# Kernel optimization log

Hardware: AMD Instinct MI355X
Metric: run time of the kernel (lower is better)

The kernel has to match this reference:

```python
import jax, jax.numpy as jnp
import numpy as np

D_MODEL = 1024
FFN_H = 4096
N_EXPERTS = 8
TOP_K = 2
AUX_COEFF = 0.01


def setup_inputs() -> dict:
    key = jax.random.key(0)
    k_x, k_r, k_w1, k_w2 = jax.random.split(key, 4)
    x = jax.random.normal(k_x, (2, 2048, D_MODEL), dtype=jnp.float32)
    Wr = jax.random.normal(k_r, (N_EXPERTS, D_MODEL), dtype=jnp.float32) * (D_MODEL ** -0.5)
    W1 = jax.random.normal(k_w1, (N_EXPERTS, FFN_H, D_MODEL), dtype=jnp.float32) * (D_MODEL ** -0.5)
    W2 = jax.random.normal(k_w2, (N_EXPERTS, D_MODEL, FFN_H), dtype=jnp.float32) * (FFN_H ** -0.5)
    return {"x": x, "Wr": Wr, "W1": W1, "W2": W2}


def reference(x, Wr, W1, W2):
    B, T, D = x.shape
    E = Wr.shape[0]
    x_flat = x.reshape(-1, D)  # (N, D)
    # Router: softmax over experts, top-k, renormalize
    router_logits = x_flat @ Wr.T  # (N, E)
    router_probs = jax.nn.softmax(router_logits, axis=-1)
    top_k_probs, top_k_indices = jax.lax.top_k(router_probs, TOP_K)
    top_k_probs = top_k_probs / (top_k_probs.sum(-1, keepdims=True) + 1e-8)
    # Dense all-expert FFN (faithful to the vectorized dispatch)
    h = jnp.einsum('nd,ehd->neh', x_flat, W1)  # (N, E, H)
    h = jax.nn.gelu(h, approximate=False)      # torch F.gelu default = erf
    out_all = jnp.einsum('neh,edh->ned', h, W2)  # (N, E, D)
    topk_out = jnp.take_along_axis(out_all, top_k_indices[:, :, None], axis=1)  # (N, K, D)
    output = (topk_out * top_k_probs[:, :, None]).sum(1)  # (N, D)
    # Load-balance aux loss (MSE to uniform)
    tokens_per_expert = router_probs.mean(0)
    aux_loss = AUX_COEFF * jnp.mean((tokens_per_expert - 1.0 / E) ** 2)
    return output.reshape(B, T, D), aux_loss
```

## Files before the change

kernel.cpp:

```cpp
#include <hip/hip_runtime.h>
#include <cstdint>
#include <cstddef>

#define N_TOK 4096
#define DM 1024
#define FH 4096
#define NE 8
#define MT_PAD 72

typedef __attribute__((ext_vector_type(8))) short short8;
typedef __attribute__((ext_vector_type(4))) float f32x4;

#define WAITV0() asm volatile("s_waitcnt vmcnt(0)" ::: "memory")

__device__ __forceinline__ unsigned short f2bf(float f) {
  unsigned u = __float_as_uint(f);
  u += 0x7fffu + ((u >> 16) & 1u);
  return (unsigned short)(u >> 16);
}

__device__ __forceinline__ float gelu_fast(float v) {
  float e = __expf(1.5957692f * v * fmaf(0.044715f, v * v, 1.0f));
  return v - v * __builtin_amdgcn_rcpf(1.0f + e);
}

__global__ void cvt_kernel(const float* __restrict__ src, unsigned short* __restrict__ dst, int n4) {
  int stride = gridDim.x * blockDim.x;
  for (int i = blockIdx.x * blockDim.x + threadIdx.x; i < n4; i += stride) {
    float4 v = reinterpret_cast<const float4*>(src)[i];
    ushort4 o;
    o.x = f2bf(v.x); o.y = f2bf(v.y); o.z = f2bf(v.z); o.w = f2bf(v.w);
    reinterpret_cast<ushort4*>(dst)[i] = o;
  }
}

__global__ void router_kernel(const float* __restrict__ x, const float* __restrict__ Wr,
                              float* __restrict__ partials, unsigned char* __restrict__ topidx,
                              float* __restrict__ pslot, unsigned short* __restrict__ xb) {
  __shared__ float sp[NE];
  int lane = threadIdx.x & 63;
  int wv = threadIdx.x >> 6;
  int token = blockIdx.x * 4 + wv;
  if (threadIdx.x < NE) sp[threadIdx.x] = 0.f;
  __syncthreads();

  const float4* xr = (const float4*)(x + (size_t)token * DM);
  ushort4* xw = (ushort4*)(xb + (size_t)token * DM);
  float acc[NE];
#pragma unroll
  for (int e = 0; e < NE; e++) acc[e] = 0.f;
#pragma unroll
  for (int d = lane; d < DM / 4; d += 64) {
    float4 xv = xr[d];
    ushort4 o;
    o.x = f2bf(xv.x); o.y = f2bf(xv.y); o.z = f2bf(xv.z); o.w = f2bf(xv.w);
    xw[d] = o;
#pragma unroll
    for (int e = 0; e < NE; e++) {
      float4 wv4 = ((const float4*)(Wr + e * DM))[d];
      acc[e] += xv.x * wv4.x + xv.y * wv4.y + xv.z * wv4.z + xv.w * wv4.w;
    }
  }
#pragma unroll
  for (int e = 0; e < NE; e++) {
#pragma unroll
    for (int off = 32; off > 0; off >>= 1) acc[e] += __shfl_xor(acc[e], off);
  }
  if (lane == 0) {
    float m = acc[0];
#pragma unroll
    for (int e = 1; e < NE; e++) m = fmaxf(m, acc[e]);
    float p[NE];
    float s = 0.f;
#pragma unroll
    for (int e = 0; e < NE; e++) { p[e] = expf(acc[e] - m); s += p[e]; }
    float inv = 1.f / s;
#pragma unroll
    for (int e = 0; e < NE; e++) p[e] *= inv;
    int i1 = 0;
#pragma unroll
    for (int e = 1; e < NE; e++) if (p[e] > p[i1]) i1 = e;
    int i2 = (i1 == 0) ? 1 : 0;
#pragma unroll
    for (int e = 0; e < NE; e++) if (e != i1 && p[e] > p[i2]) i2 = e;
    float denom = p[i1] + p[i2] + 1e-8f;
    topidx[token] = (unsigned char)(i1 | (i2 << 4));
    pslot[2 * token]     = p[i1] / denom;
    pslot[2 * token + 1] = p[i2] / denom;
#pragma unroll
    for (int e = 0; e < NE; e++) atomicAdd(&sp[e], p[e]);
  }
  __syncthreads();
  if (threadIdx.x < NE) partials[blockIdx.x * NE + threadIdx.x] = sp[threadIdx.x];
}

__global__ void scatter_kernel(const unsigned char* __restrict__ topidx,
                               int* __restrict__ counts, int* __restrict__ lists) {
  int token = blockIdx.x * blockDim.x + threadIdx.x;
  int lane = threadIdx.x & 63;
  unsigned char packed = topidx[token];
#pragma unroll
  for (int c = 0; c < 2; c++) {
    int myexp = (c == 0) ? (packed & 15) : (packed >> 4);
    int slot = 2 * token + c;
#pragma unroll
    for (int e = 0; e < NE; e++) {
      unsigned long long mask = __ballot(myexp == e);
      int cnt = __popcll(mask);
      if (cnt) {
        int base = 0;
        if (lane == 0) base = atomicAdd(&counts[e], cnt);
        base = __shfl(base, 0);
        if (myexp == e) {
          int mypos = base + __popcll(mask & ((1ull << lane) - 1ull));
          lists[e * N_TOK + mypos] = slot;
        }
      }
    }
  }
}

__global__ void tilemap_kernel(const int* __restrict__ counts, int* __restrict__ prefix,
                               int2* __restrict__ tilemap) {
  if (threadIdx.x != 0) return;
  int off = 0, tix = 0;
  for (int e = 0; e < NE; e++) {
    prefix[e] = off;
    int c = counts[e];
    int ntile = (c + 127) >> 7;
    for (int m = 0; m < ntile; m++) { tilemap[tix].x = e; tilemap[tix].y = m; tix++; }
    off += c;
  }
  prefix[NE] = off;
  while (tix < MT_PAD) { tilemap[tix].x = -1; tilemap[tix].y = 0; tix++; }
}

__global__ void aux_kernel(const float* __restrict__ partials, int nblk,
                           float* __restrict__ aux_out) {
  __shared__ float sp[NE];
  if (threadIdx.x < NE) sp[threadIdx.x] = 0.f;
  __syncthreads();
  float s = 0.f;
  for (int i = threadIdx.x; i < nblk * NE; i += 256) s += partials[i];
  atomicAdd(&sp[threadIdx.x & 7], s);
  __syncthreads();
  if (threadIdx.x == 0) {
    float a = 0.f;
#pragma unroll
    for (int e = 0; e < NE; e++) {
      float tpe = sp[e] * (1.0f / N_TOK);
      float d = tpe - 1.0f / NE;
      a += d * d;
    }
    aux_out[0] = 0.01f * (a * (1.0f / NE));
  }
}

template <int KDIM, int NT, bool IS_GEMM1>
__global__ __launch_bounds__(256, 3) void moe_gemm128(
    const unsigned short* __restrict__ Aglob,
    const unsigned short* __restrict__ Bglob,
    const int* __restrict__ prefix,
    const int2* __restrict__ tilemap,
    const int* __restrict__ lists,
    const float* __restrict__ pslot,
    unsigned short* __restrict__ hb,
    float* __restrict__ out) {
  const int NWG = NT * MT_PAD;
  int wg = blockIdx.x;
  int flat = (wg & 7) * (NWG >> 3) + (wg >> 3);
  int nt = flat % NT;
  int tix = flat / NT;

  int2 tm = tilemap[tix];
  if (tm.x < 0) return;
  int e = tm.x, mt = tm.y;
  int base = prefix[e];
  int cnt  = prefix[e + 1] - base;
  const int* list = lists + e * N_TOK;
  const unsigned short* B = Bglob + (size_t)e * (size_t)(NT * 128) * KDIM;

  __shared__ unsigned short As[128 * 64];
  __shared__ unsigned short Bs[128 * 64];

  int tid = threadIdx.x, wid = tid >> 6, lane = tid & 63;
  int wr = wid >> 1, wc = wid & 1;

  int swz = (((lane & 7) ^ (lane >> 3)) << 3);
  const unsigned short* ap[4];
  const unsigned short* bp[4];
#pragma unroll
  for (int i = 0; i < 4; i++) {
    int c = i * 4 + wid;
    int r = c * 8 + (lane >> 3);
    int p = mt * 128 + r;
    int pc = p < cnt ? p : cnt - 1;
    int arow = IS_GEMM1 ? (list[pc] >> 1) : (base + pc);
    ap[i] = Aglob + (size_t)arow * KDIM + swz;
    bp[i] = B + (size_t)(nt * 128 + r) * KDIM + swz;
  }

  f32x4 acc[4][4];
#pragma unroll
  for (int m = 0; m < 4; m++)
#pragma unroll
    for (int n = 0; n < 4; n++) acc[m][n] = (f32x4){0.f, 0.f, 0.f, 0.f};

  const int T = KDIM / 64;
  for (int t = 0; t < T; ++t) {
    if (t > 0) __syncthreads();
#pragma unroll
    for (int i = 0; i < 4; i++) {
      int c = i * 4 + wid;
      __builtin_amdgcn_global_load_lds((const void*)(ap[i] + (size_t)t * 64),
                                       (void*)(&As[c * 512]), 16, 0, 0);
      __builtin_amdgcn_global_load_lds((const void*)(bp[i] + (size_t)t * 64),
                                       (void*)(&Bs[c * 512]), 16, 0, 0);
    }
    WAITV0();
    __syncthreads();
#pragma unroll
    for (int ks = 0; ks < 2; ks++) {
      short8 aF[4], bF[4];
#pragma unroll
      for (int m = 0; m < 4; m++) {
        int row = wr * 64 + m * 16 + (lane & 15);
        int cswz = (ks * 64 + ((lane >> 4) << 4)) ^ ((row & 7) << 4);
        aF[m] = *(const short8*)((const char*)As + row * 128 + cswz);
      }
#pragma unroll
      for (int n = 0; n < 4; n++) {
        int row = wc * 64 + n * 16 + (lane & 15);
        int cswz = (ks * 64 + ((lane >> 4) << 4)) ^ ((row & 7) << 4);
        bF[n] = *(const short8*)((const char*)Bs + row * 128 + cswz);
      }
      __builtin_amdgcn_s_setprio(1);
#pragma unroll
      for (int m = 0; m < 4; m++)
#pragma unroll
        for (int n = 0; n < 4; n++)
          acc[m][n] = __builtin_amdgcn_mfma_f32_16x16x32_bf16(aF[m], bF[n], acc[m][n], 0, 0, 0);
      __builtin_amdgcn_s_setprio(0);
    }
  }

  int colpart = nt * 128 + wc * 64 + (lane & 15);
#pragma unroll
  for (int m = 0; m < 4; m++) {
#pragma unroll
    for (int rr = 0; rr < 4; rr++) {
      int p = mt * 128 + wr * 64 + m * 16 + (lane >> 4) * 4 + rr;
      if (p < cnt) {
        if (IS_GEMM1) {
          size_t rowbase = (size_t)(base + p) * FH + colpart;
#pragma unroll
          for (int n = 0; n < 4; n++)
            hb[rowbase + n * 16] = f2bf(gelu_fast(acc[m][n][rr]));
        } else {
          int slot = list[p];
          float sc = pslot[slot];
          size_t rowbase = (size_t)(slot >> 1) * DM + colpart;
#pragma unroll
          for (int n = 0; n < 4; n++) atomicAdd(&out[rowbase + n * 16], sc * acc[m][n][rr]);
        }
      }
    }
  }
}

extern "C" void kernel_launch(void* const* d_in, const int* in_sizes, int n_in,
                              void* d_out, int out_size, void* d_ws, size_t ws_size,
                              hipStream_t stream) {
  const float* x  = (const float*)d_in[0];
  const float* Wr = (const float*)d_in[1];
  const float* W1 = (const float*)d_in[2];
  const float* W2 = (const float*)d_in[3];
  float* out = (float*)d_out;

  char* ws = (char*)d_ws;
  int*   counts   = (int*)(ws + 0);
  int*   prefix   = (int*)(ws + 64);
  unsigned char* topidx = (unsigned char*)(ws + 128);
  int2*  tilemap  = (int2*)(ws + 4352);
  float* pslot    = (float*)(ws + 8192);
  float* partials = (float*)(ws + 40960);
  int*   lists    = (int*)(ws + 73728);
  unsigned short* xb  = (unsigned short*)(ws + 204800);
  unsigned short* w1b = (unsigned short*)(ws + 204800 + 8388608);
  unsigned short* w2b = (unsigned short*)(ws + 204800 + 8388608 + 67108864);
  unsigned short* hb  = (unsigned short*)(ws + 204800 + 8388608 + 2ull * 67108864);
  (void)in_sizes; (void)n_in; (void)ws_size;

  hipMemsetAsync(counts, 0, 32, stream);
  hipMemsetAsync(out, 0, (size_t)out_size * sizeof(float), stream);

  cvt_kernel<<<2048, 256, 0, stream>>>(W1, w1b, NE * FH * DM / 4);
  cvt_kernel<<<2048, 256, 0, stream>>>(W2, w2b, NE * DM * FH / 4);

  router_kernel<<<N_TOK / 4, 256, 0, stream>>>(x, Wr, partials, topidx, pslot, xb);
  scatter_kernel<<<N_TOK / 256, 256, 0, stream>>>(topidx, counts, lists);
  tilemap_kernel<<<1, 64, 0, stream>>>(counts, prefix, tilemap);
  aux_kernel<<<1, 256, 0, stream>>>(partials, N_TOK / 4, out + (size_t)N_TOK * DM);

  moe_gemm128<DM, FH / 128, true><<<(FH / 128) * MT_PAD, 256, 0, stream>>>(
      xb, w1b, prefix, tilemap, lists, pslot, hb, nullptr);
  moe_gemm128<FH, DM / 128, false><<<(DM / 128) * MT_PAD, 256, 0, stream>>>(
      hb, w2b, prefix, tilemap, lists, pslot, nullptr, out);
}
```

Measured before the change: 321.1 us.

## Double-buffer LDS tiles in MoE GEMM and split-K the second expert GEMM

The expert GEMM kernel now double-buffers its A and B LDS tiles. The next K-slice is prefetched with global_load_lds while MFMAs run on the current slice, which removes one barrier-and-wait stall per iteration. The kernel also gains a split-K template parameter, used with KZ=4 for the down-projection GEMM so that it launches four times as many workgroups over shorter K ranges. This improves CU fill for a grid that is otherwise small. In exchange, LDS use per block doubles, the minimum-occupancy launch bound is dropped, and each output element receives more atomic adds.

```diff
diff --git a/kernel.cpp b/kernel.cpp
--- a/kernel.cpp
+++ b/kernel.cpp
@@ -156,8 +156,8 @@
   }
 }
 
-template <int KDIM, int NT, bool IS_GEMM1>
-__global__ __launch_bounds__(256, 3) void moe_gemm128(
+template <int KDIM, int NT, int KZ, bool IS_GEMM1>
+__global__ __launch_bounds__(256) void moe_gemm128(
     const unsigned short* __restrict__ Aglob,
     const unsigned short* __restrict__ Bglob,
     const int* __restrict__ prefix,
@@ -166,11 +166,12 @@
     const float* __restrict__ pslot,
     unsigned short* __restrict__ hb,
     float* __restrict__ out) {
-  const int NWG = NT * MT_PAD;
+  const int NWG = NT * MT_PAD * KZ;
   int wg = blockIdx.x;
   int flat = (wg & 7) * (NWG >> 3) + (wg >> 3);
-  int nt = flat % NT;
-  int tix = flat / NT;
+  int nt  = flat % NT;
+  int kz  = (flat / NT) % KZ;
+  int tix = flat / (NT * KZ);
 
   int2 tm = tilemap[tix];
   if (tm.x < 0) return;
@@ -180,11 +181,14 @@
   const int* list = lists + e * N_TOK;
   const unsigned short* B = Bglob + (size_t)e * (size_t)(NT * 128) * KDIM;
 
-  __shared__ unsigned short As[128 * 64];
-  __shared__ unsigned short Bs[128 * 64];
+  __shared__ unsigned short As[2 * 128 * 64];
+  __shared__ unsigned short Bs[2 * 128 * 64];
 
   int tid = threadIdx.x, wid = tid >> 6, lane = tid & 63;
   int wr = wid >> 1, wc = wid & 1;
+
+  const int KC = KDIM / KZ;
+  const int T  = KC / 64;
 
   int swz = (((lane & 7) ^ (lane >> 3)) << 3);
   const unsigned short* ap[4];
@@ -196,9 +200,20 @@
     int p = mt * 128 + r;
     int pc = p < cnt ? p : cnt - 1;
     int arow = IS_GEMM1 ? (list[pc] >> 1) : (base + pc);
-    ap[i] = Aglob + (size_t)arow * KDIM + swz;
-    bp[i] = B + (size_t)(nt * 128 + r) * KDIM + swz;
-  }
+    ap[i] = Aglob + (size_t)arow * KDIM + kz * KC + swz;
+    bp[i] = B + (size_t)(nt * 128 + r) * KDIM + kz * KC + swz;
+  }
+
+#define STAGE(buf, kt) do { \
+    _Pragma("unroll") \
+    for (int i = 0; i < 4; i++) { \
+      int c = i * 4 + wid; \
+      __builtin_amdgcn_global_load_lds((const void*)(ap[i] + (size_t)(kt) * 64), \
+                                       (void*)(&As[(buf) * 8192 + c * 512]), 16, 0, 0); \
+      __builtin_amdgcn_global_load_lds((const void*)(bp[i] + (size_t)(kt) * 64), \
+                                       (void*)(&Bs[(buf) * 8192 + c * 512]), 16, 0, 0); \
+    } \
+  } while (0)
 
   f32x4 acc[4][4];
 #pragma unroll
@@ -206,19 +221,16 @@
 #pragma unroll
     for (int n = 0; n < 4; n++) acc[m][n] = (f32x4){0.f, 0.f, 0.f, 0.f};
 
-  const int T = KDIM / 64;
+  STAGE(0, 0);
+  WAITV0();
+  __syncthreads();
+
+  int cur = 0;
   for (int t = 0; t < T; ++t) {
-    if (t > 0) __syncthreads();
-#pragma unroll
-    for (int i = 0; i < 4; i++) {
-      int c = i * 4 + wid;
-      __builtin_amdgcn_global_load_lds((const void*)(ap[i] + (size_t)t * 64),
-                                       (void*)(&As[c * 512]), 16, 0, 0);
-      __builtin_amdgcn_global_load_lds((const void*)(bp[i] + (size_t)t * 64),
-                                       (void*)(&Bs[c * 512]), 16, 0, 0);
-    }
-    WAITV0();
-    __syncthreads();
+    if (t + 1 < T) STAGE(cur ^ 1, t + 1);
+
+    const char* Ab = (const char*)&As[cur * 8192];
+    const char* Bb = (const char*)&Bs[cur * 8192];
 #pragma unroll
     for (int ks = 0; ks < 2; ks++) {
       short8 aF[4], bF[4];
@@ -226,13 +238,13 @@
       for (int m = 0; m < 4; m++) {
         int row = wr * 64 + m * 16 + (lane & 15);
         int cswz = (ks * 64 + ((lane >> 4) << 4)) ^ ((row & 7) << 4);
-        aF[m] = *(const short8*)((const char*)As + row * 128 + cswz);
+        aF[m] = *(const short8*)(Ab + row * 128 + cswz);
       }
 #pragma unroll
       for (int n = 0; n < 4; n++) {
         int row = wc * 64 + n * 16 + (lane & 15);
         int cswz = (ks * 64 + ((lane >> 4) << 4)) ^ ((row & 7) << 4);
-        bF[n] = *(const short8*)((const char*)Bs + row * 128 + cswz);
+        bF[n] = *(const short8*)(Bb + row * 128 + cswz);
       }
       __builtin_amdgcn_s_setprio(1);
 #pragma unroll
@@ -242,7 +254,11 @@
           acc[m][n] = __builtin_amdgcn_mfma_f32_16x16x32_bf16(aF[m], bF[n], acc[m][n], 0, 0, 0);
       __builtin_amdgcn_s_setprio(0);
     }
-  }
+
+    if (t + 1 < T) { WAITV0(); __syncthreads(); }
+    cur ^= 1;
+  }
+#undef STAGE
 
   int colpart = nt * 128 + wc * 64 + (lane & 15);
 #pragma unroll
@@ -302,8 +318,8 @@
   tilemap_kernel<<<1, 64, 0, stream>>>(counts, prefix, tilemap);
   aux_kernel<<<1, 256, 0, stream>>>(partials, N_TOK / 4, out + (size_t)N_TOK * DM);
 
-  moe_gemm128<DM, FH / 128, true><<<(FH / 128) * MT_PAD, 256, 0, stream>>>(
+  moe_gemm128<DM, FH / 128, 1, true><<<(FH / 128) * MT_PAD, 256, 0, stream>>>(
       xb, w1b, prefix, tilemap, lists, pslot, hb, nullptr);
-  moe_gemm128<FH, DM / 128, false><<<(DM / 128) * MT_PAD, 256, 0, stream>>>(
+  moe_gemm128<FH, DM / 128, 4, false><<<(DM / 128) * MT_PAD * 4, 256, 0, stream>>>(
       hb, w2b, prefix, tilemap, lists, pslot, nullptr, out);
 }
```

Result: slower. 426.7 us (+32.9%).
